# Kernel optimization log

Hardware: AMD Instinct MI355X
Metric: run time of the kernel (lower is better)

## Reference

```python
import jax, jax.numpy as jnp
import numpy as np
from jax import lax

D_MODEL = 1024
N_HEADS = 16
KERNEL = 3
STRIDE = 1
PAD = 1
BATCH = 32
SEQ = D_MODEL  # required by the module's reshape: seq_len must equal d_model


def setup_inputs() -> dict:
    key = jax.random.key(0)
    k1, k2, k3, k4, k5, k6 = jax.random.split(key, 6)
    query_sequences = jax.random.normal(k1, (BATCH, SEQ, D_MODEL), dtype=jnp.float32)
    key_sequences = jax.random.normal(k2, (BATCH, SEQ, D_MODEL), dtype=jnp.float32)
    value_sequences = jax.random.normal(k3, (BATCH, SEQ, D_MODEL), dtype=jnp.float32)
    key_value_sequence_lengths = jax.random.randint(k4, (BATCH,), 0, SEQ).astype(jnp.int64)
    # nn.Linear(d_model, n_heads*kernel_size) params (stored as (in, out) for x @ W)
    scale = 1.0 / np.sqrt(D_MODEL)
    Wq = jax.random.uniform(k5, (D_MODEL, N_HEADS * KERNEL), minval=-scale, maxval=scale, dtype=jnp.float32)
    bq = jax.random.uniform(k6, (N_HEADS * KERNEL,), minval=-scale, maxval=scale, dtype=jnp.float32)
    return {
        "query_sequences": query_sequences,
        "key_sequences": key_sequences,
        "value_sequences": value_sequences,
        "key_value_sequence_lengths": key_value_sequence_lengths,
        "Wq": Wq,
        "bq": bq,
    }


def reference(query_sequences, key_sequences, value_sequences, key_value_sequence_lengths, Wq, bq):
    B, S, D = query_sequences.shape
    # per-batch dynamic conv kernels from queries: (B, S, H*K) -> (B*H, D, K)
    # (valid because S == D, mirroring the torch .view)
    qk = jnp.einsum('bsd,df->bsf', query_sequences, Wq) + bq
    kernels = qk.reshape(B * N_HEADS, D, KERNEL)
    # keys as a single grouped-conv input: (1, B*D, S)
    keys = jnp.transpose(key_sequences, (0, 2, 1)).reshape(1, B * D, S)
    # grouped conv1d with groups = batch_size (each group: in=D, out=N_HEADS)
    out = lax.conv_general_dilated(
        keys, kernels,
        window_strides=(STRIDE,),
        padding=[(PAD, PAD)],
        dimension_numbers=('NCH', 'OIH', 'NCH'),
        feature_group_count=B,
    )
    return out.reshape(B, N_HEADS, S)
```

## Files before the change

### kernel.cpp

```cpp
#include <hip/hip_runtime.h>
#include <hip/hip_bf16.h>
#include <stdint.h>

typedef __attribute__((ext_vector_type(8))) short bf16x8;
typedef __attribute__((ext_vector_type(4))) float f32x4;

__device__ __forceinline__ short f2bf(float x) {
    __hip_bfloat16 h = __float2bfloat16(x);
    return __builtin_bit_cast(short, h);
}

__device__ __forceinline__ bf16x8 pack8(f32x4 a, f32x4 b) {
    bf16x8 r;
    r[0] = f2bf(a[0]); r[1] = f2bf(a[1]); r[2] = f2bf(a[2]); r[3] = f2bf(a[3]);
    r[4] = f2bf(b[0]); r[5] = f2bf(b[1]); r[6] = f2bf(b[2]); r[7] = f2bf(b[3]);
    return r;
}

#define GLDS(gp, lp) __builtin_amdgcn_global_load_lds( \
    (const __attribute__((address_space(1))) void*)(gp), \
    (__attribute__((address_space(3))) void*)(lp), 16, 0, 0)

__global__ __launch_bounds__(256) void prep_wfrag(const float* __restrict__ Wq,
                                                  short* __restrict__ wfrag) {
    int idx = blockIdx.x * 256 + threadIdx.x;
    int j    = idx & 7;
    int lane = (idx >> 3) & 63;
    int grp  = idx >> 9;
    int nf   = grp % 3;
    int ks   = grp / 3;
    int k = ks * 32 + ((lane >> 4) << 3) + j;
    int n = nf * 16 + (lane & 15);
    wfrag[idx] = f2bf(Wq[k * 48 + n]);
}

__global__ __launch_bounds__(256) void qk_gemm(const float* __restrict__ Q,
                                               const short* __restrict__ wfrag,
                                               const float* __restrict__ bq,
                                               short* __restrict__ wgtA) {
    const int l  = threadIdx.x & 63;
    const int w  = threadIdx.x >> 6;
    const int lr = l & 15;
    const int lk = l >> 4;
    const int row0 = blockIdx.x * 64 + w * 16;

    f32x4 acc[3];
    acc[0] = (f32x4){0.f, 0.f, 0.f, 0.f};
    acc[1] = acc[0];
    acc[2] = acc[0];

    const float* qbase = Q + (size_t)(row0 + lr) * 1024 + lk * 8;

    #pragma unroll 4
    for (int ks = 0; ks < 32; ++ks) {
        const float* p = qbase + ks * 32;
        f32x4 q0 = *(const f32x4*)p;
        f32x4 q1 = *(const f32x4*)(p + 4);
        bf16x8 a = pack8(q0, q1);
        const bf16x8* wp = (const bf16x8*)(wfrag + (size_t)ks * 1536 + l * 8);
        acc[0] = __builtin_amdgcn_mfma_f32_16x16x32_bf16(a, wp[0],   acc[0], 0, 0, 0);
        acc[1] = __builtin_amdgcn_mfma_f32_16x16x32_bf16(a, wp[64],  acc[1], 0, 0, 0);
        acc[2] = __builtin_amdgcn_mfma_f32_16x16x32_bf16(a, wp[128], acc[2], 0, 0, 0);
    }

    #pragma unroll
    for (int nf = 0; nf < 3; ++nf) {
        int n = nf * 16 + lr;
        float bias = bq[n];
        int t  = n / 3;
        int kk = n - t * 3;
        #pragma unroll
        for (int r = 0; r < 4; ++r) {
            int row = row0 + lk * 4 + r;
            int b   = row >> 10;
            int h   = (row >> 6) & 15;
            int sp  = row & 63;
            int dg  = sp * 2 + (t >> 3);
            int j   = t & 7;
            wgtA[(((size_t)(b * 3 + kk) * 128 + dg) << 7) + h * 8 + j] = f2bf(acc[nf][r] + bias);
        }
    }
}

__global__ __launch_bounds__(256, 4) void conv_mfma(const float* __restrict__ Key,
                                                    const short* __restrict__ wgtA,
                                                    float* __restrict__ out) {
    __shared__ char stage[4 * 9216];
    __shared__ float red[2][16][17];
    const int blk = (blockIdx.x & 7) * 128 + (blockIdx.x >> 3);
    const int st  = blk & 31;
    const int b   = blk >> 5;
    const int tid = threadIdx.x;
    const int l   = tid & 63;
    const int w   = tid >> 6;
    const int lr  = l & 15;
    const int lk  = l >> 4;
    const int ss  = w & 1;
    const int dh  = w >> 1;
    const int s0  = st << 5;

    const char* gaddr[9];
    {
        const char* keyB = (const char*)(Key + ((size_t)b << 20));
        int cb = (l & 15) << 4;
        #pragma unroll
        for (int i = 0; i < 9; ++i) {
            int grow = i * 4 + (l >> 4);
            int srow = s0 - 1 + grow;
            srow = srow < 0 ? 0 : (srow > 1023 ? 1023 : srow);
            int gb   = cb ^ ((grow & 7) << 4);
            int colb = gb + ((gb >> 7) * 1920);
            gaddr[i] = keyB + (size_t)srow * 4096 + colb;
        }
    }

    const short* wgtW = wgtA + (((size_t)b * 384 + (dh << 6) + lk) << 7) + lr * 8;
    bf16x8 aw0[3], aw1[3];
    f32x4 acc = (f32x4){0.f, 0.f, 0.f, 0.f};

    #define ALOADV(arr, tt) do{ _Pragma("unroll") \
        for (int k3 = 0; k3 < 3; ++k3) \
            arr[k3] = *(const bf16x8*)(wgtW + k3 * 16384 + (tt) * 512); }while(0)

    #define STAGEV(tt) do{ char* bb_ = stage + ((tt) & 3) * 9216; _Pragma("unroll") \
        for (int i9 = 0; i9 < 9; ++i9) GLDS(gaddr[i9] + (tt) * 128, bb_ + i9 * 1024); }while(0)

    #define ZFIX(tt) do{ \
        if (st == 0  && l < 16) *(f32x4*)(stage + ((tt)&3)*9216 + (l<<4)) = (f32x4){0.f,0.f,0.f,0.f}; \
        if (st == 31 && l < 16) *(f32x4*)(stage + ((tt)&3)*9216 + 33*256 + (l<<4)) = (f32x4){0.f,0.f,0.f,0.f}; \
        if (st == 0 || st == 31) asm volatile("s_waitcnt lgkmcnt(0)" ::: "memory"); }while(0)

    #define COMP(tt) do{ \
        const char* bb_ = stage + ((tt) & 3) * 9216; \
        _Pragma("unroll") for (int k3 = 0; k3 < 3; ++k3) { \
            int row_ = ss * 16 + lr + k3; \
            const char* rb_ = bb_ + row_ * 256; \
            int sw_ = (row_ & 7) << 4; \
            int x_  = (dh << 7) + (lk << 5); \
            f32x4 v0_ = *(const f32x4*)(rb_ + ((x_) ^ sw_)); \
            f32x4 v1_ = *(const f32x4*)(rb_ + ((x_ + 16) ^ sw_)); \
            bf16x8 a_ = ((tt) & 1) ? aw1[k3] : aw0[k3]; \
            acc = __builtin_amdgcn_mfma_f32_16x16x32_bf16(a_, pack8(v0_, v1_), acc, 0, 0, 0); \
        } }while(0)

    #define STEP(tt, NW0, NWX) do{ \
        if ((tt) < 15) { if ((tt) & 1) ALOADV(aw0, (tt)+1); else ALOADV(aw1, (tt)+1); } \
        if (w == 0) { \
            if ((tt) < 13) STAGEV((tt) + 3); \
            asm volatile("s_waitcnt vmcnt(" NW0 ")" ::: "memory"); \
            ZFIX(tt); \
        } else { \
            asm volatile("s_waitcnt vmcnt(" NWX ")" ::: "memory"); \
        } \
        __builtin_amdgcn_s_barrier(); \
        asm volatile("" ::: "memory"); \
        COMP(tt); \
        asm volatile("" ::: "memory"); \
        __builtin_amdgcn_s_barrier(); }while(0)

    if (w == 0) { STAGEV(0); STAGEV(1); STAGEV(2); }
    ALOADV(aw0, 0);

    STEP(0,  "21", "3");  STEP(1,  "21", "3");  STEP(2,  "21", "3");
    STEP(3,  "21", "3");  STEP(4,  "21", "3");  STEP(5,  "21", "3");
    STEP(6,  "21", "3");  STEP(7,  "21", "3");  STEP(8,  "21", "3");
    STEP(9,  "21", "3");  STEP(10, "21", "3");  STEP(11, "21", "3");
    STEP(12, "21", "3");  STEP(13, "12", "3");  STEP(14, "3",  "3");
    STEP(15, "0",  "0");

    #undef ALOADV
    #undef STAGEV
    #undef ZFIX
    #undef COMP
    #undef STEP

    if (dh == 1) {
        #pragma unroll
        for (int r4 = 0; r4 < 4; ++r4) red[ss][lk * 4 + r4][lr] = acc[r4];
    }
    __syncthreads();
    if (dh == 0) {
        const int s = s0 + ss * 16 + lr;
        #pragma unroll
        for (int r4 = 0; r4 < 4; ++r4) {
            int h = lk * 4 + r4;
            out[(((b << 4) + h) << 10) + s] = acc[r4] + red[ss][h][lr];
        }
    }
}

extern "C" void kernel_launch(void* const* d_in, const int* in_sizes, int n_in,
                              void* d_out, int out_size, void* d_ws, size_t ws_size,
                              hipStream_t stream) {
    const float* Q  = (const float*)d_in[0];
    const float* K  = (const float*)d_in[1];
    const float* Wq = (const float*)d_in[4];
    const float* bq = (const float*)d_in[5];
    float* outp = (float*)d_out;

    short* wfrag = (short*)d_ws;
    short* wgtA  = (short*)((char*)d_ws + 98304);

    hipLaunchKernelGGL(prep_wfrag, dim3(192),  dim3(256), 0, stream, Wq, wfrag);
    hipLaunchKernelGGL(qk_gemm,    dim3(512),  dim3(256), 0, stream, Q, wfrag, bq, wgtA);
    hipLaunchKernelGGL(conv_mfma,  dim3(1024), dim3(256), 0, stream, K, wgtA, outp);
}
```

Measured before the change: 60.21 us.

## Give each wave its own LDS staging buffer and drop block barriers in conv

Staging of key tiles into LDS moves from wave 0 filling a shared buffer for the whole block to each wave loading its own 18-row by 128-byte slice with 4-byte global_load_lds operations. This removes the two block-wide s_barriers per step, because each wave now waits only on its own vmcnt. In exchange it issues 4-byte instead of 16-byte async loads, so each wave issues more memory instructions. Rows shared between neighbouring waves are now loaded twice, and the vmcnt wait counts are retuned to match.

```diff
diff --git a/kernel.cpp b/kernel.cpp
--- a/kernel.cpp
+++ b/kernel.cpp
@@ -17,9 +17,9 @@
     return r;
 }
 
-#define GLDS(gp, lp) __builtin_amdgcn_global_load_lds( \
+#define GLDS4(gp, lp) __builtin_amdgcn_global_load_lds( \
     (const __attribute__((address_space(1))) void*)(gp), \
-    (__attribute__((address_space(3))) void*)(lp), 16, 0, 0)
+    (__attribute__((address_space(3))) void*)(lp), 4, 0, 0)
 
 __global__ __launch_bounds__(256) void prep_wfrag(const float* __restrict__ Wq,
                                                   short* __restrict__ wfrag) {
@@ -85,7 +85,7 @@
 __global__ __launch_bounds__(256, 4) void conv_mfma(const float* __restrict__ Key,
                                                     const short* __restrict__ wgtA,
                                                     float* __restrict__ out) {
-    __shared__ char stage[4 * 9216];
+    __shared__ char klds[4][4 * 2304];
     __shared__ float red[2][16][17];
     const int blk = (blockIdx.x & 7) * 128 + (blockIdx.x >> 3);
     const int st  = blk & 31;
@@ -97,80 +97,77 @@
     const int lk  = l >> 4;
     const int ss  = w & 1;
     const int dh  = w >> 1;
-    const int s0  = st << 5;
+    const int sbase = (st << 5) + (ss << 4);
 
     const char* gaddr[9];
     {
-        const char* keyB = (const char*)(Key + ((size_t)b << 20));
-        int cb = (l & 15) << 4;
+        const char* keyB = (const char*)Key + ((size_t)b << 22) + (dh << 11);
+        const int cb = (l & 31) << 2;
         #pragma unroll
         for (int i = 0; i < 9; ++i) {
-            int grow = i * 4 + (l >> 4);
-            int srow = s0 - 1 + grow;
+            int grow = 2 * i + (l >> 5);
+            int srow = sbase - 1 + grow;
             srow = srow < 0 ? 0 : (srow > 1023 ? 1023 : srow);
-            int gb   = cb ^ ((grow & 7) << 4);
-            int colb = gb + ((gb >> 7) * 1920);
-            gaddr[i] = keyB + (size_t)srow * 4096 + colb;
+            gaddr[i] = keyB + (size_t)srow * 4096 + (cb ^ ((grow & 7) << 4));
         }
     }
+    char* ldsW = &klds[w][0];
+    const bool zlo = (st == 0  && ss == 0);
+    const bool zhi = (st == 31 && ss == 1);
 
     const short* wgtW = wgtA + (((size_t)b * 384 + (dh << 6) + lk) << 7) + lr * 8;
-    bf16x8 aw0[3], aw1[3];
+    bf16x8 awA[3], awB[3];
     f32x4 acc = (f32x4){0.f, 0.f, 0.f, 0.f};
+    const f32x4 z4 = acc;
 
     #define ALOADV(arr, tt) do{ _Pragma("unroll") \
         for (int k3 = 0; k3 < 3; ++k3) \
             arr[k3] = *(const bf16x8*)(wgtW + k3 * 16384 + (tt) * 512); }while(0)
 
-    #define STAGEV(tt) do{ char* bb_ = stage + ((tt) & 3) * 9216; _Pragma("unroll") \
-        for (int i9 = 0; i9 < 9; ++i9) GLDS(gaddr[i9] + (tt) * 128, bb_ + i9 * 1024); }while(0)
-
-    #define ZFIX(tt) do{ \
-        if (st == 0  && l < 16) *(f32x4*)(stage + ((tt)&3)*9216 + (l<<4)) = (f32x4){0.f,0.f,0.f,0.f}; \
-        if (st == 31 && l < 16) *(f32x4*)(stage + ((tt)&3)*9216 + 33*256 + (l<<4)) = (f32x4){0.f,0.f,0.f,0.f}; \
-        if (st == 0 || st == 31) asm volatile("s_waitcnt lgkmcnt(0)" ::: "memory"); }while(0)
+    #define STAGEV(tt) do{ char* bb_ = ldsW + ((tt) & 3) * 2304; _Pragma("unroll") \
+        for (int i9 = 0; i9 < 9; ++i9) GLDS4(gaddr[i9] + (tt) * 128, bb_ + i9 * 256); }while(0)
+
+    #define WAITV(N) do{ asm volatile("s_waitcnt vmcnt(" N ")" ::: "memory"); \
+        __builtin_amdgcn_sched_barrier(0); }while(0)
+
+    #define ZFIXW(tt) do{ \
+        if (zlo && l < 8) *(f32x4*)(ldsW + ((tt) & 3) * 2304 + (l << 4)) = z4; \
+        if (zhi && l < 8) *(f32x4*)(ldsW + ((tt) & 3) * 2304 + 17 * 128 + (l << 4)) = z4; }while(0)
 
     #define COMP(tt) do{ \
-        const char* bb_ = stage + ((tt) & 3) * 9216; \
+        const char* bb_ = ldsW + ((tt) & 3) * 2304; \
         _Pragma("unroll") for (int k3 = 0; k3 < 3; ++k3) { \
-            int row_ = ss * 16 + lr + k3; \
-            const char* rb_ = bb_ + row_ * 256; \
+            int row_ = lr + k3; \
+            const char* rb_ = bb_ + row_ * 128; \
             int sw_ = (row_ & 7) << 4; \
-            int x_  = (dh << 7) + (lk << 5); \
-            f32x4 v0_ = *(const f32x4*)(rb_ + ((x_) ^ sw_)); \
+            int x_  = lk << 5; \
+            f32x4 v0_ = *(const f32x4*)(rb_ + (x_ ^ sw_)); \
             f32x4 v1_ = *(const f32x4*)(rb_ + ((x_ + 16) ^ sw_)); \
-            bf16x8 a_ = ((tt) & 1) ? aw1[k3] : aw0[k3]; \
+            bf16x8 a_ = ((tt) & 1) ? awB[k3] : awA[k3]; \
             acc = __builtin_amdgcn_mfma_f32_16x16x32_bf16(a_, pack8(v0_, v1_), acc, 0, 0, 0); \
         } }while(0)
 
-    #define STEP(tt, NW0, NWX) do{ \
-        if ((tt) < 15) { if ((tt) & 1) ALOADV(aw0, (tt)+1); else ALOADV(aw1, (tt)+1); } \
-        if (w == 0) { \
-            if ((tt) < 13) STAGEV((tt) + 3); \
-            asm volatile("s_waitcnt vmcnt(" NW0 ")" ::: "memory"); \
-            ZFIX(tt); \
-        } else { \
-            asm volatile("s_waitcnt vmcnt(" NWX ")" ::: "memory"); \
-        } \
-        __builtin_amdgcn_s_barrier(); \
-        asm volatile("" ::: "memory"); \
-        COMP(tt); \
-        asm volatile("" ::: "memory"); \
-        __builtin_amdgcn_s_barrier(); }while(0)
-
-    if (w == 0) { STAGEV(0); STAGEV(1); STAGEV(2); }
-    ALOADV(aw0, 0);
-
-    STEP(0,  "21", "3");  STEP(1,  "21", "3");  STEP(2,  "21", "3");
-    STEP(3,  "21", "3");  STEP(4,  "21", "3");  STEP(5,  "21", "3");
-    STEP(6,  "21", "3");  STEP(7,  "21", "3");  STEP(8,  "21", "3");
-    STEP(9,  "21", "3");  STEP(10, "21", "3");  STEP(11, "21", "3");
-    STEP(12, "21", "3");  STEP(13, "12", "3");  STEP(14, "3",  "3");
-    STEP(15, "0",  "0");
+    #define STEP(tt, NV) do{ \
+        if ((tt) < 15) { if ((tt) & 1) ALOADV(awA, (tt) + 1); else ALOADV(awB, (tt) + 1); } \
+        if ((tt) < 13) STAGEV((tt) + 3); \
+        WAITV(NV); \
+        ZFIXW(tt); \
+        COMP(tt); }while(0)
+
+    STAGEV(0);
+    ALOADV(awA, 0);
+    STAGEV(1);
+    STAGEV(2);
+
+    STEP(0,  "30");  STEP(1,  "21");  STEP(2,  "21");  STEP(3,  "21");
+    STEP(4,  "21");  STEP(5,  "21");  STEP(6,  "21");  STEP(7,  "21");
+    STEP(8,  "21");  STEP(9,  "21");  STEP(10, "21");  STEP(11, "21");
+    STEP(12, "21");  STEP(13, "12");  STEP(14, "3");   STEP(15, "0");
 
     #undef ALOADV
     #undef STAGEV
-    #undef ZFIX
+    #undef WAITV
+    #undef ZFIXW
     #undef COMP
     #undef STEP
 
@@ -180,7 +177,7 @@
     }
     __syncthreads();
     if (dh == 0) {
-        const int s = s0 + ss * 16 + lr;
+        const int s = sbase + lr;
         #pragma unroll
         for (int r4 = 0; r4 < 4; ++r4) {
             int h = lk * 4 + r4;
```

After: 62.71 us. 1.04x slower.
